# Kernel tuning notes

Measured on AMD Instinct MI355X. Metric: run time of the kernel, lower is better.

## Reference

```python
import jax, jax.numpy as jnp
import numpy as np

N = 50000
E = 800000
HID = 128
HEADS = 3
OPH = (HID + HEADS - 1) // HEADS  # 43
MID = OPH * HEADS                 # 129
OUT = 6


def _gat_layer(x, src, dst, W, a_src, a_dst, b, heads, ch, concat, num_nodes):
    # x: [N, F_in]; W: [F_in, heads*ch]; a_src/a_dst: [heads, ch]; b: [heads*ch] or [ch]
    h = (x @ W).reshape(num_nodes, heads, ch)          # [N, H, C]
    al = jnp.einsum('nhc,hc->nh', h, a_src)            # [N, H]
    ar = jnp.einsum('nhc,hc->nh', h, a_dst)            # [N, H]
    e = jax.nn.leaky_relu(al[src] + ar[dst], 0.2)      # [E, H]
    emax = jax.ops.segment_max(e, dst, num_segments=num_nodes)
    emax = jnp.where(jnp.isfinite(emax), emax, 0.0)
    ex = jnp.exp(e - emax[dst])                        # [E, H]
    denom = jax.ops.segment_sum(ex, dst, num_segments=num_nodes)
    alpha = ex / (denom[dst] + 1e-16)                  # [E, H]
    msg = h[src] * alpha[:, :, None]                   # [E, H, C]
    out = jax.ops.segment_sum(msg, dst, num_segments=num_nodes)  # [N, H, C]
    out = out.reshape(num_nodes, heads * ch) if concat else out.mean(axis=1)
    return out + b


def setup_inputs() -> dict:
    key = jax.random.key(0)
    ks = jax.random.split(key, 16)
    x = jax.random.normal(ks[0], (N, HID), dtype=jnp.float32)
    edge_index = jax.random.randint(ks[1], (2, E), 0, N, dtype=jnp.int64)
    s = 0.1
    return {
        'x': x, 'edge_index': edge_index,
        'W0': jax.random.normal(ks[2], (HID, HEADS * OPH), jnp.float32) * s,
        'a0s': jax.random.normal(ks[3], (HEADS, OPH), jnp.float32) * s,
        'a0d': jax.random.normal(ks[4], (HEADS, OPH), jnp.float32) * s,
        'b0': jnp.zeros((HEADS * OPH,), jnp.float32),
        'W1': jax.random.normal(ks[5], (MID, HEADS * OPH), jnp.float32) * s,
        'a1s': jax.random.normal(ks[6], (HEADS, OPH), jnp.float32) * s,
        'a1d': jax.random.normal(ks[7], (HEADS, OPH), jnp.float32) * s,
        'b1': jnp.zeros((HEADS * OPH,), jnp.float32),
        'W2': jax.random.normal(ks[8], (MID, OUT), jnp.float32) * s,
        'a2s': jax.random.normal(ks[9], (1, OUT), jnp.float32) * s,
        'a2d': jax.random.normal(ks[10], (1, OUT), jnp.float32) * s,
        'b2': jnp.zeros((OUT,), jnp.float32),
    }


def reference(x, edge_index, W0, a0s, a0d, b0, W1, a1s, a1d, b1, W2, a2s, a2d, b2):
    # add self loops (GATConv add_self_loops=True)
    loops = jnp.arange(N, dtype=edge_index.dtype)
    src = jnp.concatenate([edge_index[0], loops])
    dst = jnp.concatenate([edge_index[1], loops])
    h = _gat_layer(x, src, dst, W0, a0s, a0d, b0, HEADS, OPH, True, N)
    h = jax.nn.leaky_relu(h, 0.2)
    h = _gat_layer(h, src, dst, W1, a1s, a1d, b1, HEADS, OPH, True, N)
    h = jax.nn.leaky_relu(h, 0.2)
    out = _gat_layer(h, src, dst, W2, a2s, a2d, b2, 1, OUT, False, N)
    return out
```

## Files before the change

kernel.cpp:

```cpp
#include <hip/hip_runtime.h>

#define N_NODES 50000
#define N_EDGES 800000
#define ET (N_EDGES + N_NODES)
#define MID 129
#define OUTC 6
#define NB 196
#define CT 4096

typedef _Float16 half2v __attribute__((ext_vector_type(2)));
typedef _Float16 half8  __attribute__((ext_vector_type(8)));
typedef float    floatx4 __attribute__((ext_vector_type(4)));

__device__ __forceinline__ float lrelu(float x) { return x > 0.f ? x : 0.2f * x; }


__global__ void ccount_kernel(const int* __restrict__ dst, int* __restrict__ ccnt) {
    __shared__ int lh[NB];
    for (int i = threadIdx.x; i < NB; i += 256) lh[i] = 0;
    __syncthreads();
    int base = blockIdx.x * CT;
#pragma unroll 4
    for (int j = 0; j < CT; j += 256) {
        int e = base + j + threadIdx.x;
        if (e < ET) {
            int d = (e < N_EDGES) ? dst[e] : (e - N_EDGES);
            atomicAdd(&lh[d >> 8], 1);
        }
    }
    __syncthreads();
    for (int i = threadIdx.x; i < NB; i += 256) {
        int v = lh[i];
        if (v) atomicAdd(&ccnt[i], v);
    }
}

__global__ void cscan_kernel(const int* __restrict__ ccnt, int* __restrict__ cbase,
                             int* __restrict__ ccur) {
    __shared__ int buf[256];
    int t = threadIdx.x;
    buf[t] = (t < NB) ? ccnt[t] : 0;
    __syncthreads();
    for (int off = 1; off < 256; off <<= 1) {
        int v = (t >= off) ? buf[t - off] : 0;
        __syncthreads();
        buf[t] += v;
        __syncthreads();
    }
    int excl = t ? buf[t - 1] : 0;
    if (t < NB) { cbase[t] = excl; ccur[t] = excl; }
    if (t == NB - 1) cbase[NB] = buf[t];
}

__global__ void cscatter_kernel(const int* __restrict__ src, const int* __restrict__ dst,
                                int* __restrict__ ccur, unsigned int* __restrict__ cval) {
    __shared__ unsigned int staged[CT];
    __shared__ int lh[NB], lex[NB], lcur[NB], lgb[NB];
    __shared__ int sbuf[256];
    int tid = threadIdx.x;
    for (int i = tid; i < NB; i += 256) lh[i] = 0;
    __syncthreads();
    int base = blockIdx.x * CT;
    unsigned int myv[16];
    int myb[16];
    int myn = 0;
#pragma unroll
    for (int j = 0; j < 16; ++j) {
        int e = base + j * 256 + tid;
        if (e < ET) {
            int s, d;
            if (e < N_EDGES) { s = src[e]; d = dst[e]; }
            else             { s = d = e - N_EDGES; }
            int b = d >> 8;
            myv[j] = ((unsigned)b << 24) | ((unsigned)(d & 255) << 16) | (unsigned)s;
            myb[j] = b;
            atomicAdd(&lh[b], 1);
            myn = j + 1;
        }
    }
    __syncthreads();
    sbuf[tid] = (tid < NB) ? lh[tid] : 0;
    __syncthreads();
    for (int off = 1; off < 256; off <<= 1) {
        int v = (tid >= off) ? sbuf[tid - off] : 0;
        __syncthreads();
        sbuf[tid] += v;
        __syncthreads();
    }
    if (tid < NB) {
        int excl = tid ? sbuf[tid - 1] : 0;
        lex[tid] = excl;
        lcur[tid] = excl;
    }
    __syncthreads();
    for (int j = 0; j < myn; ++j) {
        int p = atomicAdd(&lcur[myb[j]], 1);
        staged[p] = myv[j];
    }
    __syncthreads();
    if (tid < NB) {
        int c = lh[tid];
        lgb[tid] = c ? atomicAdd(&ccur[tid], c) : 0;
    }
    __syncthreads();
    int tot = ET - base; if (tot > CT) tot = CT;
    for (int i = tid; i < tot; i += 256) {
        unsigned int v = staged[i];
        int b = v >> 24;
        cval[lgb[b] + (i - lex[b])] = v;
    }
}

__global__ __launch_bounds__(512)
void fine_kernel(const unsigned int* __restrict__ cval, const int* __restrict__ cbase,
                 int* __restrict__ rowp, unsigned short* __restrict__ csr_src) {
    __shared__ int h[256], cur[256], sb[256];
    int b = blockIdx.x;
    int beg = cbase[b], end = cbase[b + 1];
    int t = threadIdx.x;
    if (t < 256) h[t] = 0;
    __syncthreads();
    for (int i = beg + t; i < end; i += 512)
        atomicAdd(&h[(cval[i] >> 16) & 255], 1);
    __syncthreads();
    if (t < 256) sb[t] = h[t];
    __syncthreads();
    for (int off = 1; off < 256; off <<= 1) {
        int v = 0;
        if (t < 256 && t >= off) v = sb[t - off];
        __syncthreads();
        if (t < 256) sb[t] += v;
        __syncthreads();
    }
    if (t < 256) {
        int excl = t ? sb[t - 1] : 0;
        cur[t] = excl;
        int dstv = (b << 8) + t;
        if (dstv <= N_NODES) rowp[dstv] = beg + excl;
    }
    __syncthreads();
    for (int i = beg + t; i < end; i += 512) {
        unsigned int v = cval[i];
        int low = (v >> 16) & 255;
        int p = atomicAdd(&cur[low], 1);
        csr_src[beg + p] = (unsigned short)(v & 0xFFFFu);
    }
}

__global__ void convx_kernel(const float* __restrict__ X, _Float16* __restrict__ Xh) {
    int i = (blockIdx.x * blockDim.x + threadIdx.x) * 8;
    if (i >= N_NODES * 128) return;
    float4 a = *(const float4*)(X + i);
    float4 b = *(const float4*)(X + i + 4);
    half8 h;
    h[0] = (_Float16)a.x; h[1] = (_Float16)a.y; h[2] = (_Float16)a.z; h[3] = (_Float16)a.w;
    h[4] = (_Float16)b.x; h[5] = (_Float16)b.y; h[6] = (_Float16)b.z; h[7] = (_Float16)b.w;
    *(half8*)(Xh + i) = h;
}

__global__ void padw_kernel(const float* __restrict__ W0, const float* __restrict__ a0s,
                            const float* __restrict__ a0d, const float* __restrict__ W1,
                            const float* __restrict__ a1s, const float* __restrict__ a1d,
                            _Float16* __restrict__ Wt0, _Float16* __restrict__ Wt1,
                            float* __restrict__ w128row1) {
    const int SEG = 144 * 128;
    int i = blockIdx.x * blockDim.x + threadIdx.x;
    if (i < 2 * SEG) {
        int l = i / SEG;
        int ii = i - l * SEG;
        int n = ii >> 7, k = ii & 127;
        const float* W = l ? W1 : W0;
        const float* as = l ? a1s : a0s;
        const float* ad = l ? a1d : a0d;
        float v = 0.f;
        if (n < 129) v = W[k * MID + n];
        else if (n < 132) {
            int h = n - 129;
            float sum = 0.f;
            for (int c = 0; c < 43; ++c) sum += W[k * MID + 43 * h + c] * as[43 * h + c];
            v = sum;
        } else if (n < 135) {
            int h = n - 132;
            float sum = 0.f;
            for (int c = 0; c < 43; ++c) sum += W[k * MID + 43 * h + c] * ad[43 * h + c];
            v = sum;
        }
        (l ? Wt1 : Wt0)[ii] = (_Float16)v;
    } else if (i < 2 * SEG + 144) {
        int n = i - 2 * SEG;
        float v = 0.f;
        if (n < 129) v = W1[128 * MID + n];
        else if (n < 132) {
            int h = n - 129;
            float sum = 0.f;
            for (int c = 0; c < 43; ++c) sum += W1[128 * MID + 43 * h + c] * a1s[43 * h + c];
            v = sum;
        } else if (n < 135) {
            int h = n - 132;
            float sum = 0.f;
            for (int c = 0; c < 43; ++c) sum += W1[128 * MID + 43 * h + c] * a1d[43 * h + c];
            v = sum;
        }
        w128row1[n] = v;
    }
}

template <bool RANK1>
__global__ __launch_bounds__(256)
void gemm_mfma_kernel(const _Float16* __restrict__ Xh, const float* __restrict__ Xl,
                      const _Float16* __restrict__ Wt, const float* __restrict__ w128,
                      _Float16* __restrict__ Hm16, float* __restrict__ Hl,
                      float* __restrict__ al, float* __restrict__ ar) {
    int wave = threadIdx.x >> 6, lane = threadIdx.x & 63;
    int mt = blockIdx.x * 4 + wave;
    if (mt * 16 >= N_NODES) return;
    int t = lane & 15, quad = lane >> 4;
    int row0 = mt * 16;

    const _Float16* arow = Xh + ((size_t)(row0 + t) << 7) + quad * 8;
    half8 af[4];
#pragma unroll
    for (int kt = 0; kt < 4; ++kt) af[kt] = *(const half8*)(arow + kt * 32);

    floatx4 acc[3];
#pragma unroll
    for (int nt = 0; nt < 3; ++nt) {
        int ntile = blockIdx.y * 3 + nt;
        const _Float16* brow = Wt + ((size_t)(ntile * 16 + t) << 7) + quad * 8;
        floatx4 a = {0.f, 0.f, 0.f, 0.f};
#pragma unroll
        for (int kt = 0; kt < 4; ++kt) {
            half8 b = *(const half8*)(brow + kt * 32);
            a = __builtin_amdgcn_mfma_f32_16x16x32_f16(af[kt], b, a, 0, 0, 0);
        }
        acc[nt] = a;
    }

#pragma unroll
    for (int r = 0; r < 4; ++r) {
        int row = row0 + quad * 4 + r;
        float xl = RANK1 ? Xl[row] : 0.f;
#pragma unroll
        for (int nt = 0; nt < 3; ++nt) {
            int n = (blockIdx.y * 3 + nt) * 16 + t;
            float v = acc[nt][r];
            if (RANK1) v += xl * w128[n];
            if (n < 128) {
                Hm16[((size_t)row << 7) + n] = (_Float16)v;
            } else if (n == 128) {
                Hl[row] = v;
            } else if (n < 132) {
                al[row * 3 + (n - 129)] = v;
            } else if (n < 135) {
                ar[row * 3 + (n - 132)] = v;
            }
        }
    }
}

template <bool ACT>
__global__ void agg129_kernel(const _Float16* __restrict__ Hm16, const float* __restrict__ Hl,
                              const float* __restrict__ al, const float* __restrict__ ar,
                              const int* __restrict__ rowp, const unsigned short* __restrict__ srcs,
                              const float* __restrict__ bias, _Float16* __restrict__ Omh,
                              float* __restrict__ Ol) {
    __shared__ float4 exs[4][64];
    int lane = threadIdx.x & 63;
    int wv   = threadIdx.x >> 6;
    int wid  = blockIdx.x * 4 + wv;
    if (wid >= N_NODES) return;

    int beg = rowp[wid], end = rowp[wid + 1];
    float ard0 = ar[wid * 3], ard1 = ar[wid * 3 + 1], ard2 = ar[wid * 3 + 2];

    int g  = lane >> 4;
    int q  = lane & 15;
    int cb = 8 * q;

    bool bm0[8], bm1[8];
#pragma unroll
    for (int j = 0; j < 8; ++j) {
        bm0[j] = (cb + j) < 43;
        bm1[j] = (cb + j) < 86;
    }

    float accv[8];
#pragma unroll
    for (int j = 0; j < 8; ++j) accv[j] = 0.f;
    float acc128 = 0.f;
    float s0 = 0.f, s1 = 0.f, s2 = 0.f;
    float4* exw = exs[wv];

    for (int base = beg; base < end; base += 64) {
        int i = base + lane;
        float e0 = 0.f, e1 = 0.f, e2 = 0.f;
        int s = 0;
        if (i < end) {
            s = (int)srcs[i];
            const float* ap = al + s * 3;
            e0 = __expf(lrelu(ap[0] + ard0));
            e1 = __expf(lrelu(ap[1] + ard1));
            e2 = __expf(lrelu(ap[2] + ard2));
            s0 += e0; s1 += e1; s2 += e2;
        }
        exw[lane] = make_float4(e0, e1, e2, __int_as_float(s));
        int cnt = end - base; if (cnt > 64) cnt = 64;
        for (int tt = 0; tt < cnt; tt += 4) {
            float4 ed = exw[tt + g];
            int ss = __float_as_int(ed.w);
            half8 hv = *(const half8*)(Hm16 + ((size_t)ss << 7) + cb);
            if (q == 0) acc128 += ed.z * Hl[ss];
#pragma unroll
            for (int j = 0; j < 8; ++j) {
                float w = bm0[j] ? ed.x : (bm1[j] ? ed.y : ed.z);
                accv[j] += w * (float)hv[j];
            }
        }
    }
#pragma unroll
    for (int off = 16; off <= 32; off <<= 1) {
#pragma unroll
        for (int j = 0; j < 8; ++j) accv[j] += __shfl_xor(accv[j], off, 64);
        acc128 += __shfl_xor(acc128, off, 64);
    }
#pragma unroll
    for (int off = 32; off; off >>= 1) {
        s0 += __shfl_xor(s0, off, 64);
        s1 += __shfl_xor(s1, off, 64);
        s2 += __shfl_xor(s2, off, 64);
    }
    float d0 = 1.f / (s0 + 1e-16f);
    float d1 = 1.f / (s1 + 1e-16f);
    float d2 = 1.f / (s2 + 1e-16f);
    if (g == 0) {
        float4 bv0 = *(const float4*)(bias + cb);
        float4 bv1 = *(const float4*)(bias + cb + 4);
        float bb[8] = {bv0.x, bv0.y, bv0.z, bv0.w, bv1.x, bv1.y, bv1.z, bv1.w};
        half8 oh;
#pragma unroll
        for (int j = 0; j < 8; ++j) {
            float dv = bm0[j] ? d0 : (bm1[j] ? d1 : d2);
            float o = accv[j] * dv + bb[j];
            if (ACT) o = lrelu(o);
            oh[j] = (_Float16)o;
        }
        *(half8*)(Omh + ((size_t)wid << 7) + cb) = oh;
        if (lane == 0) {
            float o128 = acc128 * d2 + bias[128];
            if (ACT) o128 = lrelu(o128);
            Ol[wid] = o128;
        }
    }
}

__global__ void layer2_node_kernel(const _Float16* __restrict__ Omh, const float* __restrict__ Ol,
                                   const float* __restrict__ W2, const float* __restrict__ a2s,
                                   const float* __restrict__ a2d, float* __restrict__ H2,
                                   float* __restrict__ al2, float* __restrict__ ar2) {
    int lane = threadIdx.x & 63;
    int wid  = blockIdx.x * 4 + (threadIdx.x >> 6);
    if (wid >= N_NODES) return;
    int c0 = 2 * lane;
    half2v xv = *(const half2v*)(Omh + ((size_t)wid << 7) + c0);
    float xx = (float)xv[0], xy = (float)xv[1];
    float x128 = Ol[wid];
    const float* w0p = W2 + c0 * OUTC;
    const float* w1p = W2 + (c0 + 1) * OUTC;
    float m = (lane == 0) ? x128 : 0.f;
    float p[OUTC];
#pragma unroll
    for (int c = 0; c < OUTC; ++c)
        p[c] = xx * w0p[c] + xy * w1p[c] + m * W2[128 * OUTC + c];
#pragma unroll
    for (int off = 32; off; off >>= 1)
#pragma unroll
        for (int c = 0; c < OUTC; ++c) p[c] += __shfl_xor(p[c], off, 64);
    float sl = 0.f, sr = 0.f;
#pragma unroll
    for (int c = 0; c < OUTC; ++c) { sl += p[c] * a2s[c]; sr += p[c] * a2d[c]; }
    if (lane == 0) {
#pragma unroll
        for (int c = 0; c < OUTC; ++c) H2[wid * OUTC + c] = p[c];
        al2[wid] = sl;
        ar2[wid] = sr;
    }
}

__global__ void agg6_kernel(const float* __restrict__ H2, const float* __restrict__ al2,
                            const float* __restrict__ ar2, const int* __restrict__ rowp,
                            const unsigned short* __restrict__ srcs, const float* __restrict__ b2,
                            float* __restrict__ out) {
    __shared__ float2 exs[4][64];
    int lane = threadIdx.x & 63;
    int wv   = threadIdx.x >> 6;
    int wid  = blockIdx.x * 4 + wv;
    if (wid >= N_NODES) return;
    int beg = rowp[wid], end = rowp[wid + 1];
    float ard = ar2[wid];
    int grp = lane >> 3;
    int myc = lane & 7;
    int cc  = (myc < OUTC) ? myc : 0;
    float ssum = 0.f, acc = 0.f;
    float2* exw = exs[wv];
    for (int base = beg; base < end; base += 64) {
        int i = base + lane;
        float ex = 0.f;
        int s = 0;
        if (i < end) {
            s = (int)srcs[i];
            ex = __expf(lrelu(al2[s] + ard));
            ssum += ex;
        }
        exw[lane] = make_float2(ex, __int_as_float(s));
        int cnt = end - base; if (cnt > 64) cnt = 64;
        for (int t = 0; t < cnt; t += 8) {
            float2 ed = exw[t + grp];
            int ss = __float_as_int(ed.y);
            acc += ed.x * H2[ss * OUTC + cc];
        }
    }
    acc += __shfl_xor(acc, 8, 64);
    acc += __shfl_xor(acc, 16, 64);
    acc += __shfl_xor(acc, 32, 64);
#pragma unroll
    for (int off = 32; off; off >>= 1) ssum += __shfl_xor(ssum, off, 64);
    float dinv = 1.f / (ssum + 1e-16f);
    if (lane < OUTC) out[(size_t)wid * OUTC + lane] = acc * dinv + b2[lane];
}


extern "C" void kernel_launch(void* const* d_in, const int* in_sizes, int n_in,
                              void* d_out, int out_size, void* d_ws, size_t ws_size,
                              hipStream_t stream) {
    const float* x   = (const float*)d_in[0];
    const int*   ei  = (const int*)d_in[1];
    const float* W0  = (const float*)d_in[2];
    const float* a0s = (const float*)d_in[3];
    const float* a0d = (const float*)d_in[4];
    const float* b0  = (const float*)d_in[5];
    const float* W1  = (const float*)d_in[6];
    const float* a1s = (const float*)d_in[7];
    const float* a1d = (const float*)d_in[8];
    const float* b1  = (const float*)d_in[9];
    const float* W2  = (const float*)d_in[10];
    const float* a2s = (const float*)d_in[11];
    const float* a2d = (const float*)d_in[12];
    const float* b2  = (const float*)d_in[13];
    float* out = (float*)d_out;

    char* p = (char*)d_ws;
    auto take = [&](size_t bytes) -> void* {
        void* r = (void*)p;
        p += (bytes + 255) & ~(size_t)255;
        return r;
    };
    int*            ccnt     = (int*)take((size_t)NB * 4);
    int*            cbase    = (int*)take((size_t)(NB + 1) * 4);
    int*            ccur     = (int*)take((size_t)NB * 4);
    unsigned int*   cval     = (unsigned int*)take((size_t)ET * 4);
    int*            rowp     = (int*)take((size_t)(N_NODES + 1) * 4);
    unsigned short* csr_src  = (unsigned short*)take((size_t)ET * 2);
    float*          al       = (float*)take((size_t)N_NODES * 3 * 4);
    float*          ar       = (float*)take((size_t)N_NODES * 3 * 4);
    _Float16*       Xh16     = (_Float16*)take((size_t)N_NODES * 128 * 2);
    _Float16*       Hm16     = (_Float16*)take((size_t)N_NODES * 128 * 2);
    _Float16*       Omh      = (_Float16*)take((size_t)N_NODES * 128 * 2);
    float*          Hl       = (float*)take((size_t)N_NODES * 4);
    float*          Ol       = (float*)take((size_t)N_NODES * 4);
    _Float16*       Wt0      = (_Float16*)take((size_t)144 * 128 * 2);
    _Float16*       Wt1      = (_Float16*)take((size_t)144 * 128 * 2);
    float*          w128row1 = (float*)take((size_t)144 * 4);
    float*          H2       = (float*)take((size_t)N_NODES * OUTC * 4);

    const int* esrc = ei;
    const int* edst = ei + N_EDGES;

    hipMemsetAsync(ccnt, 0, (size_t)NB * 4, stream);
    const int cgrid = (ET + CT - 1) / CT;
    ccount_kernel<<<cgrid, 256, 0, stream>>>(edst, ccnt);
    cscan_kernel<<<1, 256, 0, stream>>>(ccnt, cbase, ccur);
    cscatter_kernel<<<cgrid, 256, 0, stream>>>(esrc, edst, ccur, cval);
    fine_kernel<<<NB, 512, 0, stream>>>(cval, cbase, rowp, csr_src);

    convx_kernel<<<(N_NODES * 128 / 8 + 255) / 256, 256, 0, stream>>>(x, Xh16);
    padw_kernel<<<(2 * 144 * 128 + 144 + 255) / 256, 256, 0, stream>>>(
        W0, a0s, a0d, W1, a1s, a1d, Wt0, Wt1, w128row1);

    const dim3 gemm_grid((N_NODES / 16 + 3) / 4, 3);
    const int  node_grid = (N_NODES + 3) / 4;

    gemm_mfma_kernel<false><<<gemm_grid, 256, 0, stream>>>(Xh16, Ol, Wt0, w128row1, Hm16, Hl, al, ar);
    agg129_kernel<true><<<node_grid, 256, 0, stream>>>(Hm16, Hl, al, ar, rowp, csr_src, b0, Omh, Ol);

    gemm_mfma_kernel<true><<<gemm_grid, 256, 0, stream>>>(Omh, Ol, Wt1, w128row1, Hm16, Hl, al, ar);
    agg129_kernel<true><<<node_grid, 256, 0, stream>>>(Hm16, Hl, al, ar, rowp, csr_src, b1, Omh, Ol);

    layer2_node_kernel<<<node_grid, 256, 0, stream>>>(Omh, Ol, W2, a2s, a2d, H2, al, ar);
    agg6_kernel<<<node_grid, 256, 0, stream>>>(H2, al, ar, rowp, csr_src, b2, out);
}
```

Measured before the change: 305.8 us.

## Fuse fp16 input conversion into GEMM and layer-2 projection into aggregation

Drops the standalone fp32-to-fp16 conversion kernel and has the first GEMM read fp32 x directly, converting in registers. It also folds the layer-2 node projection (W2 matvec plus the attention logits) into the epilogue of the second aggregation kernel. That removes the layer-2 node kernel and the Omh/Ol round trip through memory. The first GEMM now reads twice the input bytes, once per N-tile column block, instead of fp16. The fused epilogue adds per-lane W2 loads and shuffles.

```diff
diff --git a/kernel.cpp b/kernel.cpp
--- a/kernel.cpp
+++ b/kernel.cpp
@@ -145,17 +145,6 @@
         int p = atomicAdd(&cur[low], 1);
         csr_src[beg + p] = (unsigned short)(v & 0xFFFFu);
     }
-}
-
-__global__ void convx_kernel(const float* __restrict__ X, _Float16* __restrict__ Xh) {
-    int i = (blockIdx.x * blockDim.x + threadIdx.x) * 8;
-    if (i >= N_NODES * 128) return;
-    float4 a = *(const float4*)(X + i);
-    float4 b = *(const float4*)(X + i + 4);
-    half8 h;
-    h[0] = (_Float16)a.x; h[1] = (_Float16)a.y; h[2] = (_Float16)a.z; h[3] = (_Float16)a.w;
-    h[4] = (_Float16)b.x; h[5] = (_Float16)b.y; h[6] = (_Float16)b.z; h[7] = (_Float16)b.w;
-    *(half8*)(Xh + i) = h;
 }
 
 __global__ void padw_kernel(const float* __restrict__ W0, const float* __restrict__ a0s,
@@ -205,9 +194,10 @@
     }
 }
 
-template <bool RANK1>
+template <bool SRC32, bool RANK1>
 __global__ __launch_bounds__(256)
-void gemm_mfma_kernel(const _Float16* __restrict__ Xh, const float* __restrict__ Xl,
+void gemm_mfma_kernel(const float* __restrict__ X32, const _Float16* __restrict__ Xh,
+                      const float* __restrict__ Xl,
                       const _Float16* __restrict__ Wt, const float* __restrict__ w128,
                       _Float16* __restrict__ Hm16, float* __restrict__ Hl,
                       float* __restrict__ al, float* __restrict__ ar) {
@@ -217,10 +207,25 @@
     int t = lane & 15, quad = lane >> 4;
     int row0 = mt * 16;
 
-    const _Float16* arow = Xh + ((size_t)(row0 + t) << 7) + quad * 8;
     half8 af[4];
-#pragma unroll
-    for (int kt = 0; kt < 4; ++kt) af[kt] = *(const half8*)(arow + kt * 32);
+    if (SRC32) {
+        const float* arow = X32 + ((size_t)(row0 + t) << 7) + quad * 8;
+#pragma unroll
+        for (int kt = 0; kt < 4; ++kt) {
+            float4 a0 = *(const float4*)(arow + kt * 32);
+            float4 a1 = *(const float4*)(arow + kt * 32 + 4);
+            half8 h;
+            h[0] = (_Float16)a0.x; h[1] = (_Float16)a0.y;
+            h[2] = (_Float16)a0.z; h[3] = (_Float16)a0.w;
+            h[4] = (_Float16)a1.x; h[5] = (_Float16)a1.y;
+            h[6] = (_Float16)a1.z; h[7] = (_Float16)a1.w;
+            af[kt] = h;
+        }
+    } else {
+        const _Float16* arow = Xh + ((size_t)(row0 + t) << 7) + quad * 8;
+#pragma unroll
+        for (int kt = 0; kt < 4; ++kt) af[kt] = *(const half8*)(arow + kt * 32);
+    }
 
     floatx4 acc[3];
 #pragma unroll
@@ -258,12 +263,15 @@
     }
 }
 
-template <bool ACT>
+template <bool ACT, bool L2EPI>
 __global__ void agg129_kernel(const _Float16* __restrict__ Hm16, const float* __restrict__ Hl,
                               const float* __restrict__ al, const float* __restrict__ ar,
                               const int* __restrict__ rowp, const unsigned short* __restrict__ srcs,
                               const float* __restrict__ bias, _Float16* __restrict__ Omh,
-                              float* __restrict__ Ol) {
+                              float* __restrict__ Ol,
+                              const float* __restrict__ W2, const float* __restrict__ a2s,
+                              const float* __restrict__ a2d, float* __restrict__ H2,
+                              float* __restrict__ al2, float* __restrict__ ar2) {
     __shared__ float4 exs[4][64];
     int lane = threadIdx.x & 63;
     int wv   = threadIdx.x >> 6;
@@ -336,53 +344,55 @@
         float4 bv0 = *(const float4*)(bias + cb);
         float4 bv1 = *(const float4*)(bias + cb + 4);
         float bb[8] = {bv0.x, bv0.y, bv0.z, bv0.w, bv1.x, bv1.y, bv1.z, bv1.w};
-        half8 oh;
+        float o[8];
 #pragma unroll
         for (int j = 0; j < 8; ++j) {
             float dv = bm0[j] ? d0 : (bm1[j] ? d1 : d2);
-            float o = accv[j] * dv + bb[j];
-            if (ACT) o = lrelu(o);
-            oh[j] = (_Float16)o;
-        }
-        *(half8*)(Omh + ((size_t)wid << 7) + cb) = oh;
+            o[j] = accv[j] * dv + bb[j];
+            if (ACT) o[j] = lrelu(o[j]);
+        }
+        float o128 = 0.f;
         if (lane == 0) {
-            float o128 = acc128 * d2 + bias[128];
+            o128 = acc128 * d2 + bias[128];
             if (ACT) o128 = lrelu(o128);
-            Ol[wid] = o128;
-        }
-    }
-}
-
-__global__ void layer2_node_kernel(const _Float16* __restrict__ Omh, const float* __restrict__ Ol,
-                                   const float* __restrict__ W2, const float* __restrict__ a2s,
-                                   const float* __restrict__ a2d, float* __restrict__ H2,
-                                   float* __restrict__ al2, float* __restrict__ ar2) {
-    int lane = threadIdx.x & 63;
-    int wid  = blockIdx.x * 4 + (threadIdx.x >> 6);
-    if (wid >= N_NODES) return;
-    int c0 = 2 * lane;
-    half2v xv = *(const half2v*)(Omh + ((size_t)wid << 7) + c0);
-    float xx = (float)xv[0], xy = (float)xv[1];
-    float x128 = Ol[wid];
-    const float* w0p = W2 + c0 * OUTC;
-    const float* w1p = W2 + (c0 + 1) * OUTC;
-    float m = (lane == 0) ? x128 : 0.f;
-    float p[OUTC];
-#pragma unroll
-    for (int c = 0; c < OUTC; ++c)
-        p[c] = xx * w0p[c] + xy * w1p[c] + m * W2[128 * OUTC + c];
-#pragma unroll
-    for (int off = 32; off; off >>= 1)
-#pragma unroll
-        for (int c = 0; c < OUTC; ++c) p[c] += __shfl_xor(p[c], off, 64);
-    float sl = 0.f, sr = 0.f;
-#pragma unroll
-    for (int c = 0; c < OUTC; ++c) { sl += p[c] * a2s[c]; sr += p[c] * a2d[c]; }
-    if (lane == 0) {
-#pragma unroll
-        for (int c = 0; c < OUTC; ++c) H2[wid * OUTC + c] = p[c];
-        al2[wid] = sl;
-        ar2[wid] = sr;
+        }
+        if (!L2EPI) {
+            half8 oh;
+#pragma unroll
+            for (int j = 0; j < 8; ++j) oh[j] = (_Float16)o[j];
+            *(half8*)(Omh + ((size_t)wid << 7) + cb) = oh;
+            if (lane == 0) Ol[wid] = o128;
+        } else {
+            float pr[OUTC];
+#pragma unroll
+            for (int c = 0; c < OUTC; ++c) pr[c] = 0.f;
+#pragma unroll
+            for (int j = 0; j < 8; ++j) {
+                const float* wr = W2 + (cb + j) * OUTC;
+                float ov = o[j];
+#pragma unroll
+                for (int c = 0; c < OUTC; ++c) pr[c] += ov * wr[c];
+            }
+            if (lane == 0) {
+#pragma unroll
+                for (int c = 0; c < OUTC; ++c) pr[c] += o128 * W2[128 * OUTC + c];
+            }
+#pragma unroll
+            for (int off = 1; off < 16; off <<= 1)
+#pragma unroll
+                for (int c = 0; c < OUTC; ++c) pr[c] += __shfl_xor(pr[c], off, 64);
+            if (lane == 0) {
+                float sl = 0.f, sr = 0.f;
+#pragma unroll
+                for (int c = 0; c < OUTC; ++c) {
+                    H2[wid * OUTC + c] = pr[c];
+                    sl += pr[c] * a2s[c];
+                    sr += pr[c] * a2d[c];
+                }
+                al2[wid] = sl;
+                ar2[wid] = sr;
+            }
+        }
     }
 }
 
@@ -462,7 +472,6 @@
     unsigned short* csr_src  = (unsigned short*)take((size_t)ET * 2);
     float*          al       = (float*)take((size_t)N_NODES * 3 * 4);
     float*          ar       = (float*)take((size_t)N_NODES * 3 * 4);
-    _Float16*       Xh16     = (_Float16*)take((size_t)N_NODES * 128 * 2);
     _Float16*       Hm16     = (_Float16*)take((size_t)N_NODES * 128 * 2);
     _Float16*       Omh      = (_Float16*)take((size_t)N_NODES * 128 * 2);
     float*          Hl       = (float*)take((size_t)N_NODES * 4);
@@ -471,6 +480,8 @@
     _Float16*       Wt1      = (_Float16*)take((size_t)144 * 128 * 2);
     float*          w128row1 = (float*)take((size_t)144 * 4);
     float*          H2       = (float*)take((size_t)N_NODES * OUTC * 4);
+    float*          al2      = (float*)take((size_t)N_NODES * 4);
+    float*          ar2      = (float*)take((size_t)N_NODES * 4);
 
     const int* esrc = ei;
     const int* edst = ei + N_EDGES;
@@ -482,19 +493,23 @@
     cscatter_kernel<<<cgrid, 256, 0, stream>>>(esrc, edst, ccur, cval);
     fine_kernel<<<NB, 512, 0, stream>>>(cval, cbase, rowp, csr_src);
 
-    convx_kernel<<<(N_NODES * 128 / 8 + 255) / 256, 256, 0, stream>>>(x, Xh16);
     padw_kernel<<<(2 * 144 * 128 + 144 + 255) / 256, 256, 0, stream>>>(
         W0, a0s, a0d, W1, a1s, a1d, Wt0, Wt1, w128row1);
 
     const dim3 gemm_grid((N_NODES / 16 + 3) / 4, 3);
     const int  node_grid = (N_NODES + 3) / 4;
 
-    gemm_mfma_kernel<false><<<gemm_grid, 256, 0, stream>>>(Xh16, Ol, Wt0, w128row1, Hm16, Hl, al, ar);
-    agg129_kernel<true><<<node_grid, 256, 0, stream>>>(Hm16, Hl, al, ar, rowp, csr_src, b0, Omh, Ol);
-
-    gemm_mfma_kernel<true><<<gemm_grid, 256, 0, stream>>>(Omh, Ol, Wt1, w128row1, Hm16, Hl, al, ar);
-    agg129_kernel<true><<<node_grid, 256, 0, stream>>>(Hm16, Hl, al, ar, rowp, csr_src, b1, Omh, Ol);
-
-    layer2_node_kernel<<<node_grid, 256, 0, stream>>>(Omh, Ol, W2, a2s, a2d, H2, al, ar);
-    agg6_kernel<<<node_grid, 256, 0, stream>>>(H2, al, ar, rowp, csr_src, b2, out);
-}
+    gemm_mfma_kernel<true, false><<<gemm_grid, 256, 0, stream>>>(
+        x, (const _Float16*)nullptr, Ol, Wt0, w128row1, Hm16, Hl, al, ar);
+    agg129_kernel<true, false><<<node_grid, 256, 0, stream>>>(
+        Hm16, Hl, al, ar, rowp, csr_src, b0, Omh, Ol,
+        nullptr, nullptr, nullptr, nullptr, nullptr, nullptr);
+
+    gemm_mfma_kernel<false, true><<<gemm_grid, 256, 0, stream>>>(
+        (const float*)nullptr, Omh, Ol, Wt1, w128row1, Hm16, Hl, al, ar);
+    agg129_kernel<true, true><<<node_grid, 256, 0, stream>>>(
+        Hm16, Hl, al, ar, rowp, csr_src, b1, (_Float16*)nullptr, (float*)nullptr,
+        W2, a2s, a2d, H2, al2, ar2);
+
+    agg6_kernel<<<node_grid, 256, 0, stream>>>(H2, al2, ar2, rowp, csr_src, b2, out);
+}
```

Result: faster. 299.3 us (-2.1%).
